# Kernel optimization log

Measured on AMD Instinct MI355X. Metric: run time of the kernel, lower is better.

Reference implementation:

```python
import jax, jax.numpy as jnp
import numpy as np


def _dwconv3d(x, w, b):
    # depthwise Conv3d, kernel 3, stride 1, padding 1 (SAME), groups = channels
    groups = x.shape[1]
    y = jax.lax.conv_general_dilated(
        x, w, window_strides=(1, 1, 1), padding='SAME',
        feature_group_count=groups,
        dimension_numbers=('NCDHW', 'OIDHW', 'NCDHW'))
    return y + b[None, :, None, None, None]


def setup_inputs() -> dict:
    key = jax.random.key(0)
    ks = jax.random.split(key, 8)
    B, C, K, D, H, W = 4, 64, 64, 16, 64, 64
    sc = 0.1
    return {
        'x_q': jax.random.normal(ks[0], (B, C, D, H, W), jnp.float32),
        'x_kv': jax.random.normal(ks[1], (B, K, D, H, W), jnp.float32),
        'wq': jax.random.normal(ks[2], (C, 1, 3, 3, 3), jnp.float32) * sc,
        'bq': jax.random.normal(ks[3], (C,), jnp.float32) * sc,
        'wk': jax.random.normal(ks[4], (K, 1, 3, 3, 3), jnp.float32) * sc,
        'bk': jax.random.normal(ks[5], (K,), jnp.float32) * sc,
        'wv': jax.random.normal(ks[6], (K, 1, 3, 3, 3), jnp.float32) * sc,
        'bv': jax.random.normal(ks[7], (K,), jnp.float32) * sc,
    }


def reference(x_q, x_kv, wq, bq, wk, bk, wv, bv):
    q = _dwconv3d(x_q, wq, bq)   # [B,C,D,H,W]
    k = _dwconv3d(x_kv, wk, bk)  # [B,K,D,H,W]
    v = _dwconv3d(x_kv, wv, bv)  # [B,K,D,H,W]
    B, C = q.shape[:2]
    K = k.shape[1]
    qf = q.reshape(B, C, -1)     # [B,C,S]
    kf = k.reshape(B, K, -1)     # [B,K,S]
    vf = v.reshape(B, K, -1)     # [B,K,S]
    attn = jnp.einsum('bcs,bks->bck', qf, kf) / jnp.sqrt(jnp.asarray(K, qf.dtype))
    attn = jax.nn.softmax(attn, axis=-1)           # [B,C,K]
    n = int(0.1 * C)
    at = attn.transpose(0, 2, 1)                   # [B,K,C]
    _, idx = jax.lax.top_k(at, n)                  # [B,K,n] indices into C
    mask = jnp.sum(jax.nn.one_hot(idx, C, dtype=attn.dtype), axis=-2)  # [B,K,C]
    attn_m = attn * mask.transpose(0, 2, 1)        # [B,C,K], NOT renormalized
    out = jnp.einsum('bck,bks->bcs', attn_m, vf).reshape(q.shape)
    return x_q + out, attn_m
```

## Files before the change

### kernel.cpp

```cpp
#include <hip/hip_runtime.h>
#include <math.h>

#define BB   4
#define CC   64
#define KK   64
#define DDim 16
#define HDim 64
#define WDim 64
#define SS   (DDim*HDim*WDim)
#define PLANE (HDim*WDim)
#define NCH2 64
#define TOPN 6
#define RSTR 68

typedef __attribute__((ext_vector_type(8))) short bf16x8;
typedef __attribute__((ext_vector_type(4))) float f32x4;

__device__ __forceinline__ unsigned cvt_pk_bf16(float lo, float hi) {
    unsigned r;
    asm("v_cvt_pk_bf16_f32 %0, %1, %2" : "=v"(r) : "v"(lo), "v"(hi));
    return r;
}
__device__ __forceinline__ float bf2f(unsigned short u) {
    union { unsigned u; float f; } v; v.u = ((unsigned)u) << 16; return v.f;
}

__global__ __launch_bounds__(256) void conv_hp3(
    const float* __restrict__ xq, const float* __restrict__ xkv,
    const float* __restrict__ wq, const float* __restrict__ bq,
    const float* __restrict__ wk, const float* __restrict__ bk,
    const float* __restrict__ wv, const float* __restrict__ bv,
    unsigned short* __restrict__ qo, unsigned short* __restrict__ ko,
    unsigned short* __restrict__ vo)
{
    __shared__ float ring[4][34*RSTR];

    int bid  = blockIdx.x;
    int work = (bid & 7) * 128 + (bid >> 3);
    int t  = work >> 9;
    int b  = (work >> 7) & 3;
    int c  = (work >> 1) & 63;
    int hh = work & 1;
    int g0 = hh << 5;

    const float* src = (t ? xkv : xq) + (size_t)(b*CC + c) * SS;
    float wA[27], wB[27], bA, bB;
    if (t == 0) {
        #pragma unroll
        for (int i = 0; i < 27; ++i) { wA[i] = wq[c*27 + i]; wB[i] = 0.f; }
        bA = bq[c]; bB = 0.f;
    } else {
        #pragma unroll
        for (int i = 0; i < 27; ++i) { wA[i] = wk[c*27 + i]; wB[i] = wv[c*27 + i]; }
        bA = bk[c]; bB = bv[c];
    }
    unsigned short* dA = (t ? ko : qo) + (size_t)(b*CC + c) * SS;
    unsigned short* dB = vo + (size_t)(b*CC + c) * SS;

    const int tid  = threadIdx.x;
    const int lane = tid & 63;
    const int wg   = tid & 7;
    const int w0   = wg << 3;
    const int hl   = tid >> 3;

    float4 stg[3];
#define SLOAD(p) {                                                             \
    const int p_ = (p);                                                        \
    const bool pv_ = (p_ >= 0 && p_ < DDim);                                   \
    _Pragma("unroll")                                                          \
    for (int i_ = 0; i_ < 3; ++i_) {                                           \
        const int fidx_ = i_*256 + tid;                                        \
        const int row_  = fidx_ >> 4;                                          \
        const int gy_   = g0 - 1 + row_;                                       \
        float4 v_ = make_float4(0.f,0.f,0.f,0.f);                              \
        if (pv_ && fidx_ < 544 && gy_ >= 0 && gy_ < HDim)                      \
            v_ = *(const float4*)(src + (size_t)p_*PLANE + gy_*WDim            \
                                  + (fidx_ & 15)*4);                           \
        stg[i_] = v_;                                                          \
    } }
#define SWRITE(p) {                                                            \
    float* R_ = ring[(p) & 3];                                                 \
    _Pragma("unroll")                                                          \
    for (int i_ = 0; i_ < 3; ++i_) {                                           \
        const int fidx_ = i_*256 + tid;                                        \
        if (fidx_ < 544)                                                       \
            *(float4*)&R_[(fidx_ >> 4)*RSTR + (fidx_ & 15)*4] = stg[i_];       \
    } }

#define COMPUTE_D(dd, DOB) {                                                   \
    float accA[8], accB[8];                                                    \
    _Pragma("unroll")                                                          \
    for (int j = 0; j < 8; ++j) { accA[j] = bA; accB[j] = bB; }                \
    _Pragma("unroll")                                                          \
    for (int dz = 0; dz < 3; ++dz) {                                           \
        const float* R = ring[((dd) + dz + 3) & 3];         \
        _Pragma("unroll")                                                      \
        for (int dy = 0; dy < 3; ++dy) {                                       \
            const int base_ = (hl + dy)*RSTR;                                  \
            float4 a0 = *(const float4*)&R[base_ + w0];                        \
            float4 a1 = *(const float4*)&R[base_ + w0 + 4];                    \
            float lh = __shfl(a1.w, lane - 1, 64);        \
            float rh = __shfl(a0.x, lane + 1, 64);       \
            float r[10];                                                       \
            r[0] = wg       ? lh : 0.f;                                        \
            r[9] = (wg < 7) ? rh : 0.f;                                        \
            r[1]=a0.x; r[2]=a0.y; r[3]=a0.z; r[4]=a0.w;                        \
            r[5]=a1.x; r[6]=a1.y; r[7]=a1.z; r[8]=a1.w;                        \
            const float ca0 = wA[dz*9 + dy*3 + 0];                             \
            const float ca1 = wA[dz*9 + dy*3 + 1];                             \
            const float ca2 = wA[dz*9 + dy*3 + 2];                             \
            const float cb0 = wB[dz*9 + dy*3 + 0];                             \
            const float cb1 = wB[dz*9 + dy*3 + 1];                             \
            const float cb2 = wB[dz*9 + dy*3 + 2];                             \
            _Pragma("unroll")                                                  \
            for (int j = 0; j < 8; ++j) {                                      \
                float sA = fmaf(ca0, r[j],   accA[j]);                         \
                sA       = fmaf(ca1, r[j+1], sA);                              \
                accA[j]  = fmaf(ca2, r[j+2], sA);                              \
                if (DOB) {                                                     \
                    float sB = fmaf(cb0, r[j],   accB[j]);                     \
                    sB       = fmaf(cb1, r[j+1], sB);                          \
                    accB[j]  = fmaf(cb2, r[j+2], sB);                          \
                }                                                              \
            }                                                                  \
        }                                                                      \
    }                                                                          \
    const int off = (dd)*PLANE + (g0 + hl)*WDim + w0;                          \
    uint2 pkA;                                                                 \
    pkA.x = cvt_pk_bf16(accA[0], accA[1]);                                     \
    pkA.y = cvt_pk_bf16(accA[2], accA[3]);                                     \
    uint2 pkA2;                                                                \
    pkA2.x = cvt_pk_bf16(accA[4], accA[5]);                                    \
    pkA2.y = cvt_pk_bf16(accA[6], accA[7]);                                    \
    *(uint2*)&dA[off]     = pkA;                                               \
    *(uint2*)&dA[off + 4] = pkA2;                                              \
    if (DOB) {                                                                 \
        uint2 pkB, pkB2;                                                       \
        pkB.x  = cvt_pk_bf16(accB[0], accB[1]);                                \
        pkB.y  = cvt_pk_bf16(accB[2], accB[3]);                                \
        pkB2.x = cvt_pk_bf16(accB[4], accB[5]);                                \
        pkB2.y = cvt_pk_bf16(accB[6], accB[7]);                                \
        *(uint2*)&dB[off]     = pkB;                                           \
        *(uint2*)&dB[off + 4] = pkB2;                                          \
    } }

    SLOAD(-1); SWRITE(-1);
    SLOAD(0);  SWRITE(0);
    SLOAD(1);  SWRITE(1);
    __syncthreads();

    if (t == 0) {
        for (int d = 0; d < DDim; ++d) {
            if (d < DDim - 1) SLOAD(d + 2);
            COMPUTE_D(d, 0);
            if (d < DDim - 1) SWRITE(d + 2);
            __syncthreads();
        }
    } else {
        for (int d = 0; d < DDim; ++d) {
            if (d < DDim - 1) SLOAD(d + 2);
            COMPUTE_D(d, 1);
            if (d < DDim - 1) SWRITE(d + 2);
            __syncthreads();
        }
    }
#undef SLOAD
#undef SWRITE
#undef COMPUTE_D
}

__global__ __launch_bounds__(256) void gemm1_mfma(
    const unsigned short* __restrict__ qb, const unsigned short* __restrict__ kb,
    float* __restrict__ part)
{
    __shared__ unsigned short lq[64*136];
    __shared__ unsigned short lk[64*136];

    int bid   = blockIdx.x;
    int b     = bid >> 6;
    int chunk = bid & 63;
    int tid   = threadIdx.x;
    int lane  = tid & 63;
    int wid   = tid >> 6;
    int c0    = wid << 4;
    int lr    = lane & 15;
    int kq    = lane >> 4;

    const unsigned short* qsrc = qb + (size_t)b*CC*SS;
    const unsigned short* ksrc = kb + (size_t)b*KK*SS;

    f32x4 acc[4];
    #pragma unroll
    for (int j = 0; j < 4; ++j) acc[j] = (f32x4){0.f, 0.f, 0.f, 0.f};

    const int sbase = chunk << 10;
    for (int sc = 0; sc < 8; ++sc) {
        const int s0 = sbase + (sc << 7);
        __syncthreads();
        #pragma unroll
        for (int it = 0; it < 8; ++it) {
            const int idx  = it*256 + tid;
            const int tile = idx >> 10;
            const int row  = (idx >> 4) & 63;
            const int ch8  = idx & 15;
            const unsigned short* s_ = (tile ? ksrc : qsrc) + (size_t)row*SS + s0 + ch8*8;
            unsigned short* d_ = (tile ? lk : lq) + row*136 + ch8*8;
            *(uint4*)d_ = *(const uint4*)s_;
        }
        __syncthreads();
        #pragma unroll
        for (int ss = 0; ss < 4; ++ss) {
            const int scol = ss*32 + kq*8;
            bf16x8 a = *(const bf16x8*)&lq[(c0 + lr)*136 + scol];
            #pragma unroll
            for (int j = 0; j < 4; ++j) {
                bf16x8 bv = *(const bf16x8*)&lk[(j*16 + lr)*136 + scol];
                acc[j] = __builtin_amdgcn_mfma_f32_16x16x32_bf16(a, bv, acc[j], 0, 0, 0);
            }
        }
    }

    float* pb = part + ((size_t)(b*NCH2 + chunk)) * (CC*KK);
    #pragma unroll
    for (int j = 0; j < 4; ++j)
        #pragma unroll
        for (int r = 0; r < 4; ++r)
            pb[(c0 + kq*4 + r)*KK + j*16 + lr] = acc[j][r];
}

__global__ __launch_bounds__(256) void reduce_attn(
    const float* __restrict__ part, float* __restrict__ attn)
{
    int bid = blockIdx.x;
    int b = bid >> 6, c = bid & 63;
    int tid = threadIdx.x;
    int k = tid & 63, g = tid >> 6;
    float s = 0.f;
    for (int ch = g; ch < NCH2; ch += 4)
        s += part[(size_t)(b*NCH2 + ch)*(CC*KK) + c*KK + k];
    __shared__ float red[256];
    red[tid] = s;
    __syncthreads();
    if (tid < 64) {
        float tot = red[tid] + red[tid+64] + red[tid+128] + red[tid+192];
        attn[b*CC*KK + c*KK + tid] = tot * 0.125f;
    }
}

__global__ __launch_bounds__(64) void softmax_topk(
    const float* __restrict__ attn, float* __restrict__ attn_m)
{
    __shared__ float p[64*65];
    int b = blockIdx.x;
    int t = threadIdx.x;
    for (int i = 0; i < 64; ++i) p[i*65 + t] = attn[b*4096 + i*64 + t];
    __syncthreads();
    float m = -1e30f;
    for (int k = 0; k < 64; ++k) m = fmaxf(m, p[t*65 + k]);
    float sum = 0.f;
    for (int k = 0; k < 64; ++k) { float e = expf(p[t*65+k] - m); p[t*65+k] = e; sum += e; }
    float inv = 1.f / sum;
    for (int k = 0; k < 64; ++k) p[t*65+k] *= inv;
    __syncthreads();
    unsigned long long chosen = 0ull;
    #pragma unroll
    for (int pass = 0; pass < TOPN; ++pass) {
        float best = -1.f; int bi = 0;
        for (int c2 = 0; c2 < 64; ++c2) {
            float v = p[c2*65 + t];
            if (!((chosen >> c2) & 1ull) && v > best) { best = v; bi = c2; }
        }
        chosen |= 1ull << bi;
    }
    for (int c2 = 0; c2 < 64; ++c2) {
        float v = p[c2*65 + t];
        attn_m[b*4096 + c2*64 + t] = ((chosen >> c2) & 1ull) ? v : 0.f;
    }
}

__global__ __launch_bounds__(256) void gemm2_out(
    const float* __restrict__ attn_m, const unsigned short* __restrict__ v,
    const float* __restrict__ xq, float* __restrict__ out)
{
    __shared__ float amt[64][68];
    __shared__ float vt[64][132];
    int bid = blockIdx.x;
    int b  = bid >> 7;
    int ch = bid & 127;
    int tid = threadIdx.x;
    for (int i = 0; i < 16; ++i) {
        int idx = i*256 + tid;
        amt[idx & 63][idx >> 6] = attn_m[b*4096 + idx];
    }
    int c0 = (tid >> 4) * 4;
    int s0 = (tid & 15) * 8;
    const unsigned short* vb = v + (size_t)b*KK*SS;
    const float* xb = xq + (size_t)b*CC*SS;
    float* ob = out + (size_t)b*CC*SS;
    int sb0 = ch * 512;
    for (int st = 0; st < 4; ++st) {
        int sb = sb0 + st*128;
        __syncthreads();
        #pragma unroll
        for (int i = 0; i < 4; ++i) {
            int idx = i*256 + tid;
            int k   = idx >> 4;
            int s8  = (idx & 15) * 8;
            uint4 pk = *(const uint4*)&vb[(size_t)k*SS + sb + s8];
            float* dst = &vt[k][s8];
            dst[0] = bf2f((unsigned short)(pk.x & 0xffff));
            dst[1] = bf2f((unsigned short)(pk.x >> 16));
            dst[2] = bf2f((unsigned short)(pk.y & 0xffff));
            dst[3] = bf2f((unsigned short)(pk.y >> 16));
            dst[4] = bf2f((unsigned short)(pk.z & 0xffff));
            dst[5] = bf2f((unsigned short)(pk.z >> 16));
            dst[6] = bf2f((unsigned short)(pk.w & 0xffff));
            dst[7] = bf2f((unsigned short)(pk.w >> 16));
        }
        __syncthreads();
        float acc[4][8] = {};
        #pragma unroll 8
        for (int k = 0; k < 64; ++k) {
            float4 a  = *(const float4*)&amt[k][c0];
            float4 v0 = *(const float4*)&vt[k][s0];
            float4 v1 = *(const float4*)&vt[k][s0+4];
            float av[4] = {a.x,a.y,a.z,a.w};
            float vv[8] = {v0.x,v0.y,v0.z,v0.w,v1.x,v1.y,v1.z,v1.w};
            #pragma unroll
            for (int i = 0; i < 4; ++i)
                #pragma unroll
                for (int j = 0; j < 8; ++j)
                    acc[i][j] = fmaf(av[i], vv[j], acc[i][j]);
        }
        #pragma unroll
        for (int i = 0; i < 4; ++i) {
            int off = (c0+i)*SS + sb + s0;
            float4 x0 = *(const float4*)&xb[off];
            float4 x1 = *(const float4*)&xb[off+4];
            *(float4*)&ob[off]   = make_float4(acc[i][0]+x0.x, acc[i][1]+x0.y,
                                               acc[i][2]+x0.z, acc[i][3]+x0.w);
            *(float4*)&ob[off+4] = make_float4(acc[i][4]+x1.x, acc[i][5]+x1.y,
                                               acc[i][6]+x1.z, acc[i][7]+x1.w);
        }
    }
}

extern "C" void kernel_launch(void* const* d_in, const int* in_sizes, int n_in,
                              void* d_out, int out_size, void* d_ws, size_t ws_size,
                              hipStream_t stream)
{
    const float* xq  = (const float*)d_in[0];
    const float* xkv = (const float*)d_in[1];
    const float* wq  = (const float*)d_in[2];
    const float* bq  = (const float*)d_in[3];
    const float* wk  = (const float*)d_in[4];
    const float* bk  = (const float*)d_in[5];
    const float* wv  = (const float*)d_in[6];
    const float* bv  = (const float*)d_in[7];
    float* out = (float*)d_out;

    unsigned short* k_ws = (unsigned short*)d_ws;
    unsigned short* v_ws = k_ws + (size_t)BB*KK*SS;
    float* part = (float*)(v_ws + (size_t)BB*KK*SS);
    float* attn = part + (size_t)BB*NCH2*CC*KK;

    unsigned short* q_bf = (unsigned short*)out;
    float* attn_m = out + (size_t)BB*CC*SS;

    conv_hp3   <<<2*BB*CC*2, 256, 0, stream>>>(xq, xkv, wq, bq, wk, bk, wv, bv,
                                               q_bf, k_ws, v_ws);
    gemm1_mfma <<<BB*NCH2,   256, 0, stream>>>(q_bf, k_ws, part);
    reduce_attn<<<BB*CC,     256, 0, stream>>>(part, attn);
    softmax_topk<<<BB,        64, 0, stream>>>(attn, attn_m);
    gemm2_out  <<<BB*128,    256, 0, stream>>>(attn_m, v_ws, xq, out);
}
```

Before: 144.8 us.

## Replace LDS ring buffer in depthwise conv with register-rotated plane windows

The conv kernel drops its shared-memory ring of input planes and barriers. Each thread now loads its own three rows (with halo) straight from global memory into registers and rotates three register windows along depth. Blocks shrink to 128 threads covering 16 rows, with twice as many blocks, and stores become single 16-byte writes. This removes LDS traffic and __syncthreads, at the cost of about three times more global row loads (relying on cache), higher register pressure, and a fully unrolled depth loop.

```diff
diff --git a/kernel.cpp b/kernel.cpp
--- a/kernel.cpp
+++ b/kernel.cpp
@@ -11,7 +11,6 @@
 #define PLANE (HDim*WDim)
 #define NCH2 64
 #define TOPN 6
-#define RSTR 68
 
 typedef __attribute__((ext_vector_type(8))) short bf16x8;
 typedef __attribute__((ext_vector_type(4))) float f32x4;
@@ -25,7 +24,7 @@
     union { unsigned u; float f; } v; v.u = ((unsigned)u) << 16; return v.f;
 }
 
-__global__ __launch_bounds__(256) void conv_hp3(
+__global__ __launch_bounds__(128) void conv_reg(
     const float* __restrict__ xq, const float* __restrict__ xkv,
     const float* __restrict__ wq, const float* __restrict__ bq,
     const float* __restrict__ wk, const float* __restrict__ bk,
@@ -33,15 +32,13 @@
     unsigned short* __restrict__ qo, unsigned short* __restrict__ ko,
     unsigned short* __restrict__ vo)
 {
-    __shared__ float ring[4][34*RSTR];
-
     int bid  = blockIdx.x;
-    int work = (bid & 7) * 128 + (bid >> 3);
-    int t  = work >> 9;
-    int b  = (work >> 7) & 3;
-    int c  = (work >> 1) & 63;
-    int hh = work & 1;
-    int g0 = hh << 5;
+    int work = (bid & 7) * 256 + (bid >> 3);
+    int t  = work >> 10;
+    int b  = (work >> 8) & 3;
+    int c  = (work >> 2) & 63;
+    int hs = work & 3;
+    int g0 = hs << 4;
 
     const float* src = (t ? xkv : xq) + (size_t)(b*CC + c) * SS;
     float wA[27], wB[27], bA, bB;
@@ -62,111 +59,108 @@
     const int wg   = tid & 7;
     const int w0   = wg << 3;
     const int hl   = tid >> 3;
-
-    float4 stg[3];
-#define SLOAD(p) {                                                             \
-    const int p_ = (p);                                                        \
-    const bool pv_ = (p_ >= 0 && p_ < DDim);                                   \
+    const int y    = g0 + hl;
+
+    float4 stg[3][2];
+    float  W0[3][10], W1[3][10], W2[3][10];
+
+#define GLOAD(p) {                                                             \
     _Pragma("unroll")                                                          \
-    for (int i_ = 0; i_ < 3; ++i_) {                                           \
-        const int fidx_ = i_*256 + tid;                                        \
-        const int row_  = fidx_ >> 4;                                          \
-        const int gy_   = g0 - 1 + row_;                                       \
-        float4 v_ = make_float4(0.f,0.f,0.f,0.f);                              \
-        if (pv_ && fidx_ < 544 && gy_ >= 0 && gy_ < HDim)                      \
-            v_ = *(const float4*)(src + (size_t)p_*PLANE + gy_*WDim            \
-                                  + (fidx_ & 15)*4);                           \
-        stg[i_] = v_;                                                          \
+    for (int rr_ = 0; rr_ < 3; ++rr_) {                                        \
+        const int gy_ = y - 1 + rr_;                                           \
+        float4 a0_ = make_float4(0.f,0.f,0.f,0.f), a1_ = a0_;                  \
+        if ((p) < DDim && gy_ >= 0 && gy_ < HDim) {                            \
+            const float* bp_ = src + (size_t)(p)*PLANE + gy_*WDim + w0;        \
+            a0_ = *(const float4*)(bp_);                                       \
+            a1_ = *(const float4*)(bp_ + 4);                                   \
+        }                                                                      \
+        stg[rr_][0] = a0_; stg[rr_][1] = a1_;                                  \
     } }
-#define SWRITE(p) {                                                            \
-    float* R_ = ring[(p) & 3];                                                 \
+
+#define CONSUME(W) {                                                           \
     _Pragma("unroll")                                                          \
-    for (int i_ = 0; i_ < 3; ++i_) {                                           \
-        const int fidx_ = i_*256 + tid;                                        \
-        if (fidx_ < 544)                                                       \
-            *(float4*)&R_[(fidx_ >> 4)*RSTR + (fidx_ & 15)*4] = stg[i_];       \
+    for (int rr_ = 0; rr_ < 3; ++rr_) {                                        \
+        float lh_ = __shfl(stg[rr_][1].w, lane - 1, 64);                       \
+        float rh_ = __shfl(stg[rr_][0].x, lane + 1, 64);                       \
+        W[rr_][0] = wg       ? lh_ : 0.f;                                      \
+        W[rr_][9] = (wg < 7) ? rh_ : 0.f;                                      \
+        W[rr_][1]=stg[rr_][0].x; W[rr_][2]=stg[rr_][0].y;                      \
+        W[rr_][3]=stg[rr_][0].z; W[rr_][4]=stg[rr_][0].w;                      \
+        W[rr_][5]=stg[rr_][1].x; W[rr_][6]=stg[rr_][1].y;                      \
+        W[rr_][7]=stg[rr_][1].z; W[rr_][8]=stg[rr_][1].w;                      \
     } }
 
-#define COMPUTE_D(dd, DOB) {                                                   \
+#define FMAS(W, dz, DOB) {                                                     \
+    _Pragma("unroll")                                                          \
+    for (int dy_ = 0; dy_ < 3; ++dy_) {                                        \
+        const float ca0_ = wA[(dz)*9 + dy_*3 + 0];                             \
+        const float ca1_ = wA[(dz)*9 + dy_*3 + 1];                             \
+        const float ca2_ = wA[(dz)*9 + dy_*3 + 2];                             \
+        const float cb0_ = wB[(dz)*9 + dy_*3 + 0];                             \
+        const float cb1_ = wB[(dz)*9 + dy_*3 + 1];                             \
+        const float cb2_ = wB[(dz)*9 + dy_*3 + 2];                             \
+        _Pragma("unroll")                                                      \
+        for (int j_ = 0; j_ < 8; ++j_) {                                       \
+            float sA_ = fmaf(ca0_, W[dy_][j_],   accA[j_]);                    \
+            sA_       = fmaf(ca1_, W[dy_][j_+1], sA_);                         \
+            accA[j_]  = fmaf(ca2_, W[dy_][j_+2], sA_);                         \
+            if (DOB) {                                                         \
+                float sB_ = fmaf(cb0_, W[dy_][j_],   accB[j_]);                \
+                sB_       = fmaf(cb1_, W[dy_][j_+1], sB_);                     \
+                accB[j_]  = fmaf(cb2_, W[dy_][j_+2], sB_);                     \
+            }                                                                  \
+        }                                                                      \
+    } }
+
+#define STEP(dd, Wa, Wb, Wc, DOB) {                                            \
+    CONSUME(Wc);                        \
+    GLOAD((dd)+2);                       \
     float accA[8], accB[8];                                                    \
     _Pragma("unroll")                                                          \
-    for (int j = 0; j < 8; ++j) { accA[j] = bA; accB[j] = bB; }                \
-    _Pragma("unroll")                                                          \
-    for (int dz = 0; dz < 3; ++dz) {                                           \
-        const float* R = ring[((dd) + dz + 3) & 3];         \
-        _Pragma("unroll")                                                      \
-        for (int dy = 0; dy < 3; ++dy) {                                       \
-            const int base_ = (hl + dy)*RSTR;                                  \
-            float4 a0 = *(const float4*)&R[base_ + w0];                        \
-            float4 a1 = *(const float4*)&R[base_ + w0 + 4];                    \
-            float lh = __shfl(a1.w, lane - 1, 64);        \
-            float rh = __shfl(a0.x, lane + 1, 64);       \
-            float r[10];                                                       \
-            r[0] = wg       ? lh : 0.f;                                        \
-            r[9] = (wg < 7) ? rh : 0.f;                                        \
-            r[1]=a0.x; r[2]=a0.y; r[3]=a0.z; r[4]=a0.w;                        \
-            r[5]=a1.x; r[6]=a1.y; r[7]=a1.z; r[8]=a1.w;                        \
-            const float ca0 = wA[dz*9 + dy*3 + 0];                             \
-            const float ca1 = wA[dz*9 + dy*3 + 1];                             \
-            const float ca2 = wA[dz*9 + dy*3 + 2];                             \
-            const float cb0 = wB[dz*9 + dy*3 + 0];                             \
-            const float cb1 = wB[dz*9 + dy*3 + 1];                             \
-            const float cb2 = wB[dz*9 + dy*3 + 2];                             \
-            _Pragma("unroll")                                                  \
-            for (int j = 0; j < 8; ++j) {                                      \
-                float sA = fmaf(ca0, r[j],   accA[j]);                         \
-                sA       = fmaf(ca1, r[j+1], sA);                              \
-                accA[j]  = fmaf(ca2, r[j+2], sA);                              \
-                if (DOB) {                                                     \
-                    float sB = fmaf(cb0, r[j],   accB[j]);                     \
-                    sB       = fmaf(cb1, r[j+1], sB);                          \
-                    accB[j]  = fmaf(cb2, r[j+2], sB);                          \
-                }                                                              \
-            }                                                                  \
-        }                                                                      \
-    }                                                                          \
-    const int off = (dd)*PLANE + (g0 + hl)*WDim + w0;                          \
-    uint2 pkA;                                                                 \
-    pkA.x = cvt_pk_bf16(accA[0], accA[1]);                                     \
-    pkA.y = cvt_pk_bf16(accA[2], accA[3]);                                     \
-    uint2 pkA2;                                                                \
-    pkA2.x = cvt_pk_bf16(accA[4], accA[5]);                                    \
-    pkA2.y = cvt_pk_bf16(accA[6], accA[7]);                                    \
-    *(uint2*)&dA[off]     = pkA;                                               \
-    *(uint2*)&dA[off + 4] = pkA2;                                              \
+    for (int j_ = 0; j_ < 8; ++j_) { accA[j_] = bA; accB[j_] = bB; }           \
+    FMAS(Wa, 0, DOB);                                                          \
+    FMAS(Wb, 1, DOB);                                                          \
+    FMAS(Wc, 2, DOB);                                                          \
+    const int off_ = (dd)*PLANE + y*WDim + w0;                                 \
+    uint4 pkA_;                                                                \
+    pkA_.x = cvt_pk_bf16(accA[0], accA[1]);                                    \
+    pkA_.y = cvt_pk_bf16(accA[2], accA[3]);                                    \
+    pkA_.z = cvt_pk_bf16(accA[4], accA[5]);                                    \
+    pkA_.w = cvt_pk_bf16(accA[6], accA[7]);                                    \
+    *(uint4*)&dA[off_] = pkA_;                                                 \
     if (DOB) {                                                                 \
-        uint2 pkB, pkB2;                                                       \
-        pkB.x  = cvt_pk_bf16(accB[0], accB[1]);                                \
-        pkB.y  = cvt_pk_bf16(accB[2], accB[3]);                                \
-        pkB2.x = cvt_pk_bf16(accB[4], accB[5]);                                \
-        pkB2.y = cvt_pk_bf16(accB[6], accB[7]);                                \
-        *(uint2*)&dB[off]     = pkB;                                           \
-        *(uint2*)&dB[off + 4] = pkB2;                                          \
+        uint4 pkB_;                                                            \
+        pkB_.x = cvt_pk_bf16(accB[0], accB[1]);                                \
+        pkB_.y = cvt_pk_bf16(accB[2], accB[3]);                                \
+        pkB_.z = cvt_pk_bf16(accB[4], accB[5]);                                \
+        pkB_.w = cvt_pk_bf16(accB[6], accB[7]);                                \
+        *(uint4*)&dB[off_] = pkB_;                                             \
     } }
 
-    SLOAD(-1); SWRITE(-1);
-    SLOAD(0);  SWRITE(0);
-    SLOAD(1);  SWRITE(1);
-    __syncthreads();
+    #pragma unroll
+    for (int rr = 0; rr < 3; ++rr)
+        #pragma unroll
+        for (int j = 0; j < 10; ++j) W2[rr][j] = 0.f;
+    GLOAD(0); CONSUME(W0);
+    GLOAD(1);
+
+#define STEP3(dbase, DOB)                                                      \
+    STEP(dbase,     W2, W0, W1, DOB);                                          \
+    STEP((dbase)+1, W0, W1, W2, DOB);                                          \
+    STEP((dbase)+2, W1, W2, W0, DOB);
 
     if (t == 0) {
-        for (int d = 0; d < DDim; ++d) {
-            if (d < DDim - 1) SLOAD(d + 2);
-            COMPUTE_D(d, 0);
-            if (d < DDim - 1) SWRITE(d + 2);
-            __syncthreads();
-        }
+        STEP3(0, 0) STEP3(3, 0) STEP3(6, 0) STEP3(9, 0) STEP3(12, 0)
+        STEP(15, W2, W0, W1, 0);
     } else {
-        for (int d = 0; d < DDim; ++d) {
-            if (d < DDim - 1) SLOAD(d + 2);
-            COMPUTE_D(d, 1);
-            if (d < DDim - 1) SWRITE(d + 2);
-            __syncthreads();
-        }
-    }
-#undef SLOAD
-#undef SWRITE
-#undef COMPUTE_D
+        STEP3(0, 1) STEP3(3, 1) STEP3(6, 1) STEP3(9, 1) STEP3(12, 1)
+        STEP(15, W2, W0, W1, 1);
+    }
+#undef GLOAD
+#undef CONSUME
+#undef FMAS
+#undef STEP
+#undef STEP3
 }
 
 __global__ __launch_bounds__(256) void gemm1_mfma(
@@ -367,7 +361,7 @@
     unsigned short* q_bf = (unsigned short*)out;
     float* attn_m = out + (size_t)BB*CC*SS;
 
-    conv_hp3   <<<2*BB*CC*2, 256, 0, stream>>>(xq, xkv, wq, bq, wk, bk, wv, bv,
+    conv_reg   <<<2*BB*CC*4, 128, 0, stream>>>(xq, xkv, wq, bq, wk, bk, wv, bv,
                                                q_bf, k_ws, v_ws);
     gemm1_mfma <<<BB*NCH2,   256, 0, stream>>>(q_bf, k_ws, part);
     reduce_attn<<<BB*CC,     256, 0, stream>>>(part, attn);
```

Measured after the change: 147.3 us. About the same (+1.7%).
